# Kernel tuning notes

Hardware: AMD Instinct MI355X
Metric: run time of the kernel (lower is better)

Reference implementation:

```python
import jax, jax.numpy as jnp
import numpy as np

N_SRC = 50000
N_DST = 50000
N_EDGES = 800000
D_IN = 128
D_HID = 128
D_OUT = 128


def setup_inputs() -> dict:
    key = jax.random.key(0)
    ks = jax.random.split(key, 8)
    h_src = jax.random.normal(ks[0], (N_SRC, D_IN), dtype=jnp.float32)
    h_dst = jax.random.normal(ks[1], (N_DST, D_IN), dtype=jnp.float32)
    weights = jax.random.uniform(ks[2], (N_EDGES,), dtype=jnp.float32)
    edge_src = jax.random.randint(ks[3], (N_EDGES,), 0, N_SRC, dtype=jnp.int64)
    edge_dst = jax.random.randint(ks[4], (N_EDGES,), 0, N_DST, dtype=jnp.int64)
    # Xavier-uniform-ish init scaled like nn.init.xavier_uniform_(gain=sqrt(2))
    gain = float(np.sqrt(2.0))
    limQ = gain * float(np.sqrt(6.0 / (D_IN + D_HID)))
    limW = gain * float(np.sqrt(6.0 / (D_IN + D_HID + D_OUT)))
    Q_w = jax.random.uniform(ks[5], (D_HID, D_IN), minval=-limQ, maxval=limQ, dtype=jnp.float32)
    Q_b = jnp.zeros((D_HID,), dtype=jnp.float32)
    W_w = jax.random.uniform(ks[6], (D_OUT, D_IN + D_HID), minval=-limW, maxval=limW, dtype=jnp.float32)
    W_b = jnp.zeros((D_OUT,), dtype=jnp.float32)
    return {
        "h_src": h_src, "h_dst": h_dst, "weights": weights,
        "edge_src": edge_src, "edge_dst": edge_dst,
        "Q_w": Q_w, "Q_b": Q_b, "W_w": W_w, "W_b": W_b,
    }


def reference(h_src, h_dst, weights, edge_src, edge_dst, Q_w, Q_b, W_w, W_b):
    # n = relu(Q(h_src))  (dropout is identity in eval mode)
    n_src = jax.nn.relu(h_src @ Q_w.T + Q_b)                    # [N_src, H]
    w = weights.astype(jnp.float32)
    # u_mul_e + sum: weighted message aggregation per destination node
    msgs = n_src[edge_src] * w[:, None]                          # [E, H]
    n = jax.ops.segment_sum(msgs, edge_dst, num_segments=N_DST)  # [N_dst, H]
    # copy_e + sum: per-destination weight sum, clamped at 1
    ws = jax.ops.segment_sum(w, edge_dst, num_segments=N_DST)
    ws = jnp.clip(ws, 1.0, None)[:, None]                        # [N_dst, 1]
    z_in = jnp.concatenate([n / ws, h_dst], axis=1)              # [N_dst, H+D]
    z = jax.nn.relu(z_in @ W_w.T + W_b)                          # [N_dst, O]
    return z
```

## Files before the change

### kernel.cpp

```cpp
#include <hip/hip_runtime.h>
#include <hip/hip_bf16.h>

#define D 128
#define BSHIFT 8
#define BSIZE 256
#define NBUCK 196
#define CAP 6144
#define P1_EPB 4096
#define QPAD 136
#define WPAD 264

typedef __attribute__((ext_vector_type(8))) short bf16x8;
typedef __attribute__((ext_vector_type(4))) float floatx4;

__device__ __forceinline__ unsigned short f2bf(float f) {
    unsigned u = __float_as_uint(f);
    return (unsigned short)((u + 0x7FFFu + ((u >> 16) & 1u)) >> 16);
}
__device__ __forceinline__ float bf2f(unsigned short s) {
    return __uint_as_float(((unsigned)s) << 16);
}

__global__ __launch_bounds__(256)
void gemm1_mfma(const float* __restrict__ h, const float* __restrict__ Qw,
                const float* __restrict__ Qb, unsigned short* __restrict__ nsrc, int M) {
    __shared__ unsigned short Bs[128 * QPAD];
    const int tid = threadIdx.x;
    const int lane = tid & 63;
    const int wv = tid >> 6;
    const int m0 = (blockIdx.x * 4 + wv) * 16;
    const int rquad = lane >> 4;
    const int rlow = lane & 15;
    const bool active = (m0 < M);

    bf16x8 a[4];
    if (active) {
#pragma unroll
        for (int q = 0; q < 4; ++q) {
            const float* pa = h + (size_t)(m0 + rlow) * D + q * 32 + rquad * 8;
            float4 x = *(const float4*)pa;
            float4 y = *(const float4*)(pa + 4);
            bf16x8 t;
            t[0] = (short)f2bf(x.x); t[1] = (short)f2bf(x.y);
            t[2] = (short)f2bf(x.z); t[3] = (short)f2bf(x.w);
            t[4] = (short)f2bf(y.x); t[5] = (short)f2bf(y.y);
            t[6] = (short)f2bf(y.z); t[7] = (short)f2bf(y.w);
            a[q] = t;
        }
    }

#pragma unroll
    for (int c = tid; c < 4096; c += 256) {
        int row = c >> 5, col4 = (c & 31) * 4;
        float4 x = *(const float4*)(Qw + row * 128 + col4);
        ushort4 t;
        t.x = f2bf(x.x); t.y = f2bf(x.y); t.z = f2bf(x.z); t.w = f2bf(x.w);
        *(ushort4*)&Bs[row * QPAD + col4] = t;
    }
    __syncthreads();
    if (!active) return;

    floatx4 acc[8];
#pragma unroll
    for (int n = 0; n < 8; ++n) acc[n] = (floatx4)0.f;

#pragma unroll
    for (int n = 0; n < 8; ++n) {
#pragma unroll
        for (int q = 0; q < 4; ++q) {
            bf16x8 b = *(const bf16x8*)&Bs[(n * 16 + rlow) * QPAD + q * 32 + rquad * 8];
            acc[n] = __builtin_amdgcn_mfma_f32_16x16x32_bf16(a[q], b, acc[n], 0, 0, 0);
        }
    }

#pragma unroll
    for (int n = 0; n < 8; ++n) {
        int col = n * 16 + rlow;
        float bias = Qb[col];
#pragma unroll
        for (int r = 0; r < 4; ++r) {
            int row = m0 + rquad * 4 + r;
            nsrc[(size_t)row * D + col] = f2bf(fmaxf(acc[n][r] + bias, 0.f));
        }
    }
}

__global__ __launch_bounds__(256)
void pass1_bucket(const int* __restrict__ esrc, const int* __restrict__ edst,
                  const float* __restrict__ w, int* __restrict__ gcursor,
                  unsigned long long* __restrict__ staging, int E) {
    __shared__ int cnt[NBUCK];
    __shared__ int base[NBUCK];
    const int tid = threadIdx.x;
    const int e0 = blockIdx.x * P1_EPB;
    for (int i = tid; i < NBUCK; i += 256) cnt[i] = 0;
    __syncthreads();
#pragma unroll
    for (int i = 0; i < P1_EPB; i += 256) {
        int e = e0 + i + tid;
        if (e < E) atomicAdd(&cnt[edst[e] >> BSHIFT], 1);
    }
    __syncthreads();
    for (int i = tid; i < NBUCK; i += 256) {
        int c = cnt[i];
        base[i] = (c > 0) ? atomicAdd(&gcursor[i], c) : 0;
        cnt[i] = 0;
    }
    __syncthreads();
#pragma unroll
    for (int i = 0; i < P1_EPB; i += 256) {
        int e = e0 + i + tid;
        if (e < E) {
            int d = edst[e];
            int b = d >> BSHIFT;
            int pos = base[b] + atomicAdd(&cnt[b], 1);
            if (pos < CAP) {
                unsigned long long pk =
                    (unsigned long long)(unsigned)(esrc[e] | ((d & (BSIZE - 1)) << 16)) |
                    ((unsigned long long)__float_as_uint(w[e]) << 32);
                staging[(size_t)b * CAP + pos] = pk;
            }
        }
    }
}

__global__ __launch_bounds__(256)
void pass2_fill(const unsigned long long* __restrict__ staging,
                const int* __restrict__ gcursor,
                int2* __restrict__ offs2, unsigned long long* __restrict__ csr, int N) {
    __shared__ int cntA[256], sB[256], exC[256];
    const int b = blockIdx.x;
    const int tid = threadIdx.x;
    int cnt = gcursor[b];
    if (cnt > CAP) cnt = CAP;
    const int base = b * CAP;
    const unsigned long long* st = staging + (size_t)b * CAP;

    cntA[tid] = 0;
    __syncthreads();
    for (int i = tid; i < cnt; i += 256)
        atomicAdd(&cntA[(int)((st[i] >> 16) & 255)], 1);
    __syncthreads();

    int v = cntA[tid];
    sB[tid] = v;
    __syncthreads();
#pragma unroll
    for (int off = 1; off < 256; off <<= 1) {
        int t = (tid >= off) ? sB[tid - off] : 0;
        __syncthreads();
        sB[tid] += t;
        __syncthreads();
    }
    exC[tid] = sB[tid] - v;
    cntA[tid] = 0;
    __syncthreads();

    int node = b * BSIZE + tid;
    if (node < N) offs2[node] = make_int2(base + exC[tid], base + exC[tid] + v);

    for (int i = tid; i < cnt; i += 256) {
        unsigned long long pk = st[i];
        int dl = (int)((pk >> 16) & 255);
        int slot = base + exC[dl] + atomicAdd(&cntA[dl], 1);
        csr[slot] = (pk & 0xFFFFull) | (pk & 0xFFFFFFFF00000000ull);
    }
}

__global__ __launch_bounds__(256)
void gather(const unsigned long long* __restrict__ csr, const int2* __restrict__ offs2,
            const unsigned short* __restrict__ nsrc, unsigned short* __restrict__ nout, int N) {
    int node = __builtin_amdgcn_readfirstlane((int)((blockIdx.x * 256 + threadIdx.x) >> 6));
    int lane = threadIdx.x & 63;
    if (node >= N) return;
    int2 be = offs2[node];
    int beg = be.x, end = be.y;

    float a0 = 0.f, a1 = 0.f, a2 = 0.f, a3 = 0.f;
    float ws0 = 0.f, ws1 = 0.f;
    const int off2 = lane * 2;

    int i = beg;
    for (; i + 8 <= end; i += 8) {
        unsigned long long p[8];
        unsigned v[8];
        float wt[8];
#pragma unroll
        for (int j = 0; j < 8; ++j) p[j] = csr[i + j];
#pragma unroll
        for (int j = 0; j < 8; ++j) {
            wt[j] = __uint_as_float((unsigned)(p[j] >> 32));
            v[j] = *(const unsigned*)(nsrc + (size_t)(unsigned)p[j] * D + off2);
        }
#pragma unroll
        for (int j = 0; j < 8; j += 2) {
            a0 += bf2f((unsigned short)v[j]) * wt[j];
            a1 += bf2f((unsigned short)(v[j] >> 16)) * wt[j];
            a2 += bf2f((unsigned short)v[j + 1]) * wt[j + 1];
            a3 += bf2f((unsigned short)(v[j + 1] >> 16)) * wt[j + 1];
            ws0 += wt[j]; ws1 += wt[j + 1];
        }
    }
    for (; i + 4 <= end; i += 4) {
        unsigned long long p0 = csr[i + 0], p1 = csr[i + 1];
        unsigned long long p2 = csr[i + 2], p3 = csr[i + 3];
        float w0 = __uint_as_float((unsigned)(p0 >> 32));
        float w1 = __uint_as_float((unsigned)(p1 >> 32));
        float w2 = __uint_as_float((unsigned)(p2 >> 32));
        float w3 = __uint_as_float((unsigned)(p3 >> 32));
        unsigned v0 = *(const unsigned*)(nsrc + (size_t)(unsigned)p0 * D + off2);
        unsigned v1 = *(const unsigned*)(nsrc + (size_t)(unsigned)p1 * D + off2);
        unsigned v2 = *(const unsigned*)(nsrc + (size_t)(unsigned)p2 * D + off2);
        unsigned v3 = *(const unsigned*)(nsrc + (size_t)(unsigned)p3 * D + off2);
        a0 += bf2f((unsigned short)v0) * w0; a1 += bf2f((unsigned short)(v0 >> 16)) * w0;
        a2 += bf2f((unsigned short)v1) * w1; a3 += bf2f((unsigned short)(v1 >> 16)) * w1;
        a0 += bf2f((unsigned short)v2) * w2; a1 += bf2f((unsigned short)(v2 >> 16)) * w2;
        a2 += bf2f((unsigned short)v3) * w3; a3 += bf2f((unsigned short)(v3 >> 16)) * w3;
        ws0 += w0 + w2; ws1 += w1 + w3;
    }
    for (; i < end; ++i) {
        unsigned long long p = csr[i];
        float wt = __uint_as_float((unsigned)(p >> 32));
        unsigned v = *(const unsigned*)(nsrc + (size_t)(unsigned)p * D + off2);
        a0 += bf2f((unsigned short)v) * wt; a1 += bf2f((unsigned short)(v >> 16)) * wt;
        ws0 += wt;
    }

    float inv = 1.f / fmaxf(ws0 + ws1, 1.f);
    unsigned outv = (unsigned)f2bf((a0 + a2) * inv) | ((unsigned)f2bf((a1 + a3) * inv) << 16);
    *(unsigned*)(nout + (size_t)node * D + off2) = outv;
}

__global__ __launch_bounds__(256)
void gemm2_mfma(const unsigned short* __restrict__ nnorm, const float* __restrict__ hdst,
                const float* __restrict__ Ww, const float* __restrict__ Wb,
                float* __restrict__ out, int M) {
    __shared__ unsigned short Bs[128 * WPAD];
    const int tid = threadIdx.x;
    const int lane = tid & 63;
    const int wv = tid >> 6;
    const int m0 = (blockIdx.x * 4 + wv) * 16;
    const int rquad = lane >> 4;
    const int rlow = lane & 15;
    const bool active = (m0 < M);

    bf16x8 a[8];
    if (active) {
#pragma unroll
        for (int q = 0; q < 4; ++q)
            a[q] = *(const bf16x8*)(nnorm + (size_t)(m0 + rlow) * D + q * 32 + rquad * 8);
#pragma unroll
        for (int q = 4; q < 8; ++q) {
            const float* pa = hdst + (size_t)(m0 + rlow) * D + (q - 4) * 32 + rquad * 8;
            float4 x = *(const float4*)pa;
            float4 y = *(const float4*)(pa + 4);
            bf16x8 t;
            t[0] = (short)f2bf(x.x); t[1] = (short)f2bf(x.y);
            t[2] = (short)f2bf(x.z); t[3] = (short)f2bf(x.w);
            t[4] = (short)f2bf(y.x); t[5] = (short)f2bf(y.y);
            t[6] = (short)f2bf(y.z); t[7] = (short)f2bf(y.w);
            a[q] = t;
        }
    }

#pragma unroll
    for (int c = tid; c < 8192; c += 256) {
        int row = c >> 6, col4 = (c & 63) * 4;
        float4 x = *(const float4*)(Ww + row * 256 + col4);
        ushort4 t;
        t.x = f2bf(x.x); t.y = f2bf(x.y); t.z = f2bf(x.z); t.w = f2bf(x.w);
        *(ushort4*)&Bs[row * WPAD + col4] = t;
    }
    __syncthreads();
    if (!active) return;

    floatx4 acc[8];
#pragma unroll
    for (int n = 0; n < 8; ++n) acc[n] = (floatx4)0.f;

#pragma unroll
    for (int n = 0; n < 8; ++n) {
#pragma unroll
        for (int q = 0; q < 8; ++q) {
            bf16x8 b = *(const bf16x8*)&Bs[(n * 16 + rlow) * WPAD + q * 32 + rquad * 8];
            acc[n] = __builtin_amdgcn_mfma_f32_16x16x32_bf16(a[q], b, acc[n], 0, 0, 0);
        }
    }

#pragma unroll
    for (int n = 0; n < 8; ++n) {
        int col = n * 16 + rlow;
        float bias = Wb[col];
#pragma unroll
        for (int r = 0; r < 4; ++r) {
            int row = m0 + rquad * 4 + r;
            out[(size_t)row * D + col] = fmaxf(acc[n][r] + bias, 0.f);
        }
    }
}

extern "C" void kernel_launch(void* const* d_in, const int* in_sizes, int n_in,
                              void* d_out, int out_size, void* d_ws, size_t ws_size,
                              hipStream_t stream) {
    const float* h_src   = (const float*)d_in[0];
    const float* h_dst   = (const float*)d_in[1];
    const float* weights = (const float*)d_in[2];
    const int*   esrc    = (const int*)d_in[3];
    const int*   edst    = (const int*)d_in[4];
    const float* Q_w     = (const float*)d_in[5];
    const float* Q_b     = (const float*)d_in[6];
    const float* W_w     = (const float*)d_in[7];
    const float* W_b     = (const float*)d_in[8];

    const int N_SRC = in_sizes[0] / D;
    const int N_DST = in_sizes[1] / D;
    const int E     = in_sizes[2];

    char* ws = (char*)d_ws;
    int*  gcursor = (int*)(ws + 0);
    int2* offs2   = (int2*)(ws + 4096);
    unsigned long long* staging = (unsigned long long*)(ws + 409600);
    unsigned long long* csr     = (unsigned long long*)(ws + 409600 + (size_t)NBUCK * CAP * 8);
    unsigned short* nsrc16  = (unsigned short*)(ws + 409600 + 2 * (size_t)NBUCK * CAP * 8);
    unsigned short* nnorm16 = (unsigned short*)(ws + 409600 + 2 * (size_t)NBUCK * CAP * 8
                                                + (size_t)N_SRC * D * 2);

    float* out = (float*)d_out;

    hipMemsetAsync(gcursor, 0, NBUCK * sizeof(int), stream);

    gemm1_mfma<<<(N_SRC + 63) / 64, 256, 0, stream>>>(h_src, Q_w, Q_b, nsrc16, N_SRC);

    pass1_bucket<<<(E + P1_EPB - 1) / P1_EPB, 256, 0, stream>>>(esrc, edst, weights,
                                                                gcursor, staging, E);

    pass2_fill<<<NBUCK, 256, 0, stream>>>(staging, gcursor, offs2, csr, N_DST);

    gather<<<(N_DST * 64 + 255) / 256, 256, 0, stream>>>(csr, offs2, nsrc16, nnorm16, N_DST);

    gemm2_mfma<<<(N_DST + 63) / 64, 256, 0, stream>>>(nnorm16, h_dst, W_w, W_b, out, N_DST);
}
```

Before: 197.2 us.

## Fuse bucket CSR fill and neighbor gather into one LDS-based kernel

Merges the per-bucket counting-sort kernel and the per-node gather kernel into one kernel. Each block now sorts its bucket's edges into shared memory (16-bit source index plus weight) and then aggregates its destination nodes directly, so the global CSR array and offsets are never written or read back. Buckets shrink to 128 nodes so the per-bucket edge list fits in LDS. In exchange the gather runs far fewer waves (4 per block, each looping over 32 nodes), which cuts the number of in-flight random loads and may hurt latency hiding.

```diff
diff --git a/kernel.cpp b/kernel.cpp
--- a/kernel.cpp
+++ b/kernel.cpp
@@ -2,10 +2,10 @@
 #include <hip/hip_bf16.h>
 
 #define D 128
-#define BSHIFT 8
-#define BSIZE 256
-#define NBUCK 196
-#define CAP 6144
+#define BSHIFT 7
+#define BSIZE 128
+#define NBUCK 391
+#define CAP 2560
 #define P1_EPB 4096
 #define QPAD 136
 #define WPAD 264
@@ -125,110 +125,106 @@
 }
 
 __global__ __launch_bounds__(256)
-void pass2_fill(const unsigned long long* __restrict__ staging,
-                const int* __restrict__ gcursor,
-                int2* __restrict__ offs2, unsigned long long* __restrict__ csr, int N) {
-    __shared__ int cntA[256], sB[256], exC[256];
+void bucket_gather(const unsigned long long* __restrict__ staging,
+                   const int* __restrict__ gcursor,
+                   const unsigned short* __restrict__ nsrc,
+                   unsigned short* __restrict__ nout, int N) {
+    __shared__ unsigned short srcL[CAP];
+    __shared__ float wgtL[CAP];
+    __shared__ int cntA[BSIZE], begL[BSIZE], endL[BSIZE];
     const int b = blockIdx.x;
     const int tid = threadIdx.x;
-    int cnt = gcursor[b];
-    if (cnt > CAP) cnt = CAP;
-    const int base = b * CAP;
+    const int lane = tid & 63;
+    const int wv = tid >> 6;
+    int cnt = min(gcursor[b], CAP);
     const unsigned long long* st = staging + (size_t)b * CAP;
 
-    cntA[tid] = 0;
+    if (tid < BSIZE) cntA[tid] = 0;
     __syncthreads();
     for (int i = tid; i < cnt; i += 256)
-        atomicAdd(&cntA[(int)((st[i] >> 16) & 255)], 1);
-    __syncthreads();
-
-    int v = cntA[tid];
-    sB[tid] = v;
-    __syncthreads();
-#pragma unroll
-    for (int off = 1; off < 256; off <<= 1) {
-        int t = (tid >= off) ? sB[tid - off] : 0;
+        atomicAdd(&cntA[(int)((st[i] >> 16) & (BSIZE - 1))], 1);
+    __syncthreads();
+    int v = (tid < BSIZE) ? cntA[tid] : 0;
+    if (tid < BSIZE) endL[tid] = v;
+    __syncthreads();
+#pragma unroll
+    for (int off = 1; off < BSIZE; off <<= 1) {
+        int t = 0;
+        if (tid < BSIZE && tid >= off) t = endL[tid - off];
         __syncthreads();
-        sB[tid] += t;
+        if (tid < BSIZE) endL[tid] += t;
         __syncthreads();
     }
-    exC[tid] = sB[tid] - v;
-    cntA[tid] = 0;
-    __syncthreads();
-
-    int node = b * BSIZE + tid;
-    if (node < N) offs2[node] = make_int2(base + exC[tid], base + exC[tid] + v);
-
+    if (tid < BSIZE) {
+        begL[tid] = endL[tid] - v;
+        cntA[tid] = endL[tid] - v;
+    }
+    __syncthreads();
     for (int i = tid; i < cnt; i += 256) {
         unsigned long long pk = st[i];
-        int dl = (int)((pk >> 16) & 255);
-        int slot = base + exC[dl] + atomicAdd(&cntA[dl], 1);
-        csr[slot] = (pk & 0xFFFFull) | (pk & 0xFFFFFFFF00000000ull);
-    }
-}
-
-__global__ __launch_bounds__(256)
-void gather(const unsigned long long* __restrict__ csr, const int2* __restrict__ offs2,
-            const unsigned short* __restrict__ nsrc, unsigned short* __restrict__ nout, int N) {
-    int node = __builtin_amdgcn_readfirstlane((int)((blockIdx.x * 256 + threadIdx.x) >> 6));
-    int lane = threadIdx.x & 63;
-    if (node >= N) return;
-    int2 be = offs2[node];
-    int beg = be.x, end = be.y;
-
-    float a0 = 0.f, a1 = 0.f, a2 = 0.f, a3 = 0.f;
-    float ws0 = 0.f, ws1 = 0.f;
+        int dl = (int)((pk >> 16) & (BSIZE - 1));
+        int slot = atomicAdd(&cntA[dl], 1);
+        srcL[slot] = (unsigned short)(pk & 0xFFFFu);
+        wgtL[slot] = __uint_as_float((unsigned)(pk >> 32));
+    }
+    __syncthreads();
+
+    const int node0 = b << BSHIFT;
     const int off2 = lane * 2;
-
-    int i = beg;
-    for (; i + 8 <= end; i += 8) {
-        unsigned long long p[8];
-        unsigned v[8];
-        float wt[8];
-#pragma unroll
-        for (int j = 0; j < 8; ++j) p[j] = csr[i + j];
-#pragma unroll
-        for (int j = 0; j < 8; ++j) {
-            wt[j] = __uint_as_float((unsigned)(p[j] >> 32));
-            v[j] = *(const unsigned*)(nsrc + (size_t)(unsigned)p[j] * D + off2);
-        }
-#pragma unroll
-        for (int j = 0; j < 8; j += 2) {
-            a0 += bf2f((unsigned short)v[j]) * wt[j];
-            a1 += bf2f((unsigned short)(v[j] >> 16)) * wt[j];
-            a2 += bf2f((unsigned short)v[j + 1]) * wt[j + 1];
-            a3 += bf2f((unsigned short)(v[j + 1] >> 16)) * wt[j + 1];
-            ws0 += wt[j]; ws1 += wt[j + 1];
-        }
-    }
-    for (; i + 4 <= end; i += 4) {
-        unsigned long long p0 = csr[i + 0], p1 = csr[i + 1];
-        unsigned long long p2 = csr[i + 2], p3 = csr[i + 3];
-        float w0 = __uint_as_float((unsigned)(p0 >> 32));
-        float w1 = __uint_as_float((unsigned)(p1 >> 32));
-        float w2 = __uint_as_float((unsigned)(p2 >> 32));
-        float w3 = __uint_as_float((unsigned)(p3 >> 32));
-        unsigned v0 = *(const unsigned*)(nsrc + (size_t)(unsigned)p0 * D + off2);
-        unsigned v1 = *(const unsigned*)(nsrc + (size_t)(unsigned)p1 * D + off2);
-        unsigned v2 = *(const unsigned*)(nsrc + (size_t)(unsigned)p2 * D + off2);
-        unsigned v3 = *(const unsigned*)(nsrc + (size_t)(unsigned)p3 * D + off2);
-        a0 += bf2f((unsigned short)v0) * w0; a1 += bf2f((unsigned short)(v0 >> 16)) * w0;
-        a2 += bf2f((unsigned short)v1) * w1; a3 += bf2f((unsigned short)(v1 >> 16)) * w1;
-        a0 += bf2f((unsigned short)v2) * w2; a1 += bf2f((unsigned short)(v2 >> 16)) * w2;
-        a2 += bf2f((unsigned short)v3) * w3; a3 += bf2f((unsigned short)(v3 >> 16)) * w3;
-        ws0 += w0 + w2; ws1 += w1 + w3;
-    }
-    for (; i < end; ++i) {
-        unsigned long long p = csr[i];
-        float wt = __uint_as_float((unsigned)(p >> 32));
-        unsigned v = *(const unsigned*)(nsrc + (size_t)(unsigned)p * D + off2);
-        a0 += bf2f((unsigned short)v) * wt; a1 += bf2f((unsigned short)(v >> 16)) * wt;
-        ws0 += wt;
-    }
-
-    float inv = 1.f / fmaxf(ws0 + ws1, 1.f);
-    unsigned outv = (unsigned)f2bf((a0 + a2) * inv) | ((unsigned)f2bf((a1 + a3) * inv) << 16);
-    *(unsigned*)(nout + (size_t)node * D + off2) = outv;
+    for (int node = wv; node < BSIZE; node += 4) {
+        int ng = node0 + node;
+        if (ng >= N) break;
+        int beg = begL[node], end = endL[node];
+
+        float a0 = 0.f, a1 = 0.f, a2 = 0.f, a3 = 0.f;
+        float ws0 = 0.f, ws1 = 0.f;
+        int i = beg;
+        for (; i + 8 <= end; i += 8) {
+            int s[8]; float wt[8]; unsigned vv[8];
+#pragma unroll
+            for (int j = 0; j < 8; ++j) {
+                s[j] = srcL[i + j];
+                wt[j] = wgtL[i + j];
+            }
+#pragma unroll
+            for (int j = 0; j < 8; ++j)
+                vv[j] = *(const unsigned*)(nsrc + (size_t)s[j] * D + off2);
+#pragma unroll
+            for (int j = 0; j < 8; j += 2) {
+                a0 += bf2f((unsigned short)vv[j]) * wt[j];
+                a1 += bf2f((unsigned short)(vv[j] >> 16)) * wt[j];
+                a2 += bf2f((unsigned short)vv[j + 1]) * wt[j + 1];
+                a3 += bf2f((unsigned short)(vv[j + 1] >> 16)) * wt[j + 1];
+                ws0 += wt[j]; ws1 += wt[j + 1];
+            }
+        }
+        for (; i + 4 <= end; i += 4) {
+            int s0 = srcL[i], s1 = srcL[i + 1], s2 = srcL[i + 2], s3 = srcL[i + 3];
+            float w0 = wgtL[i], w1 = wgtL[i + 1], w2 = wgtL[i + 2], w3 = wgtL[i + 3];
+            unsigned v0 = *(const unsigned*)(nsrc + (size_t)s0 * D + off2);
+            unsigned v1 = *(const unsigned*)(nsrc + (size_t)s1 * D + off2);
+            unsigned v2 = *(const unsigned*)(nsrc + (size_t)s2 * D + off2);
+            unsigned v3 = *(const unsigned*)(nsrc + (size_t)s3 * D + off2);
+            a0 += bf2f((unsigned short)v0) * w0; a1 += bf2f((unsigned short)(v0 >> 16)) * w0;
+            a2 += bf2f((unsigned short)v1) * w1; a3 += bf2f((unsigned short)(v1 >> 16)) * w1;
+            a0 += bf2f((unsigned short)v2) * w2; a1 += bf2f((unsigned short)(v2 >> 16)) * w2;
+            a2 += bf2f((unsigned short)v3) * w3; a3 += bf2f((unsigned short)(v3 >> 16)) * w3;
+            ws0 += w0 + w2; ws1 += w1 + w3;
+        }
+        for (; i < end; ++i) {
+            int s = srcL[i];
+            float wt = wgtL[i];
+            unsigned vvv = *(const unsigned*)(nsrc + (size_t)s * D + off2);
+            a0 += bf2f((unsigned short)vvv) * wt;
+            a1 += bf2f((unsigned short)(vvv >> 16)) * wt;
+            ws0 += wt;
+        }
+
+        float inv = 1.f / fmaxf(ws0 + ws1, 1.f);
+        unsigned outv = (unsigned)f2bf((a0 + a2) * inv) |
+                        ((unsigned)f2bf((a1 + a3) * inv) << 16);
+        *(unsigned*)(nout + (size_t)ng * D + off2) = outv;
+    }
 }
 
 __global__ __launch_bounds__(256)
@@ -317,12 +313,10 @@
     const int E     = in_sizes[2];
 
     char* ws = (char*)d_ws;
-    int*  gcursor = (int*)(ws + 0);
-    int2* offs2   = (int2*)(ws + 4096);
-    unsigned long long* staging = (unsigned long long*)(ws + 409600);
-    unsigned long long* csr     = (unsigned long long*)(ws + 409600 + (size_t)NBUCK * CAP * 8);
-    unsigned short* nsrc16  = (unsigned short*)(ws + 409600 + 2 * (size_t)NBUCK * CAP * 8);
-    unsigned short* nnorm16 = (unsigned short*)(ws + 409600 + 2 * (size_t)NBUCK * CAP * 8
+    int* gcursor = (int*)(ws + 0);
+    unsigned long long* staging = (unsigned long long*)(ws + 4096);
+    unsigned short* nsrc16  = (unsigned short*)(ws + 4096 + (size_t)NBUCK * CAP * 8);
+    unsigned short* nnorm16 = (unsigned short*)(ws + 4096 + (size_t)NBUCK * CAP * 8
                                                 + (size_t)N_SRC * D * 2);
 
     float* out = (float*)d_out;
@@ -334,9 +328,7 @@
     pass1_bucket<<<(E + P1_EPB - 1) / P1_EPB, 256, 0, stream>>>(esrc, edst, weights,
                                                                 gcursor, staging, E);
 
-    pass2_fill<<<NBUCK, 256, 0, stream>>>(staging, gcursor, offs2, csr, N_DST);
-
-    gather<<<(N_DST * 64 + 255) / 256, 256, 0, stream>>>(csr, offs2, nsrc16, nnorm16, N_DST);
+    bucket_gather<<<NBUCK, 256, 0, stream>>>(staging, gcursor, nsrc16, nnorm16, N_DST);
 
     gemm2_mfma<<<(N_DST + 63) / 64, 256, 0, stream>>>(nnorm16, h_dst, W_w, W_b, out, N_DST);
 }
```

Measured after the change: 224.7 us. 1.14x slower.
